# Performance work log

Hardware: AMD Instinct MI355X
Metric: run time of the kernel (lower is better)

The kernel has to match this reference:

```python
import jax, jax.numpy as jnp
import numpy as np

H = 100      # hidden size
L = 4096     # sequence length


def setup_inputs() -> dict:
    key = jax.random.key(0)
    ks = jax.random.split(key, 11)
    s = 1.0 / np.sqrt(H)
    u = lambda k, sh: jax.random.uniform(k, sh, jnp.float32, -s, s)
    return {
        "input_seq": jax.random.normal(ks[0], (L,), jnp.float32),
        "W_ih_l0": u(ks[1], (4 * H, 1)),
        "W_hh_l0": u(ks[2], (4 * H, H)),
        "b_ih_l0": u(ks[3], (4 * H,)),
        "b_hh_l0": u(ks[4], (4 * H,)),
        "W_ih_l1": u(ks[5], (4 * H, H)),
        "W_hh_l1": u(ks[6], (4 * H, H)),
        "b_ih_l1": u(ks[7], (4 * H,)),
        "b_hh_l1": u(ks[8], (4 * H,)),
        "W_lin": u(ks[9], (1, H)),
        "b_lin": u(ks[10], (1,)),
    }


def _lstm_layer(x, Wih, Whh, bih, bhh):
    # x: [L, B, in] -> hs: [L, B, H]. PyTorch gate order: i, f, g, o.
    h_dim = Wih.shape[0] // 4
    b = bih + bhh

    def step(carry, xt):
        h, c = carry
        gates = xt @ Wih.T + h @ Whh.T + b          # [B, 4H]
        i, f, g, o = jnp.split(gates, 4, axis=-1)
        c = jax.nn.sigmoid(f) * c + jax.nn.sigmoid(i) * jnp.tanh(g)
        h = jax.nn.sigmoid(o) * jnp.tanh(c)
        return (h, c), h

    B = x.shape[1]
    h0 = jnp.zeros((B, h_dim), x.dtype)
    c0 = jnp.zeros((B, h_dim), x.dtype)
    _, hs = jax.lax.scan(step, (h0, c0), x)
    return hs


def reference(input_seq, W_ih_l0, W_hh_l0, b_ih_l0, b_hh_l0,
              W_ih_l1, W_hh_l1, b_ih_l1, b_hh_l1, W_lin, b_lin):
    x = input_seq.reshape(-1, 1, 1)                 # [L, B=1, 1]
    h1 = _lstm_layer(x, W_ih_l0, W_hh_l0, b_ih_l0, b_hh_l0)   # [L,1,H]
    h2 = _lstm_layer(h1, W_ih_l1, W_hh_l1, b_ih_l1, b_hh_l1)  # [L,1,H]
    preds = h2.reshape(h2.shape[0], -1) @ W_lin.T + b_lin      # [L,1]
    return preds[-1]                                 # [1]
```

## Files before the change

kernel.cpp:

```cpp
#include <hip/hip_runtime.h>

#define HH 100
#define LL 4096
#define NT 512

#define WS_H1_FLOATS (LL*128)
#define WS_NEEDED ((size_t)WS_H1_FLOATS*4 + (size_t)LL*4)

typedef float v2f __attribute__((ext_vector_type(2)));
__device__ __forceinline__ v2f fma2(v2f a, v2f b, v2f c) { return __builtin_elementwise_fma(a, b, c); }
__device__ __forceinline__ v2f v2c(float2 f) { v2f r; r.x = f.x; r.y = f.y; return r; }

__device__ __forceinline__ float sigmoidf_(float x) { return 1.0f / (1.0f + __expf(-x)); }
__device__ __forceinline__ float tanhf_(float x)    { return 1.0f - 2.0f / (__expf(2.0f * x) + 1.0f); }

#define DECLROW(n) v2f n##_0,n##_1,n##_2,n##_3,n##_4,n##_5,n##_6,n##_7,n##_8,n##_9,n##_10,n##_11, \
                       n##_12,n##_13,n##_14,n##_15,n##_16,n##_17,n##_18,n##_19,n##_20,n##_21,n##_22,n##_23,n##_24;
#define LOADROW(n, P) { const float2* q2_ = reinterpret_cast<const float2*>(P); \
  n##_0=v2c(q2_[0]);   n##_1=v2c(q2_[1]);   n##_2=v2c(q2_[2]);   n##_3=v2c(q2_[3]);   n##_4=v2c(q2_[4]); \
  n##_5=v2c(q2_[5]);   n##_6=v2c(q2_[6]);   n##_7=v2c(q2_[7]);   n##_8=v2c(q2_[8]);   n##_9=v2c(q2_[9]); \
  n##_10=v2c(q2_[10]); n##_11=v2c(q2_[11]); n##_12=v2c(q2_[12]); n##_13=v2c(q2_[13]); n##_14=v2c(q2_[14]); \
  n##_15=v2c(q2_[15]); n##_16=v2c(q2_[16]); n##_17=v2c(q2_[17]); n##_18=v2c(q2_[18]); n##_19=v2c(q2_[19]); \
  n##_20=v2c(q2_[20]); n##_21=v2c(q2_[21]); n##_22=v2c(q2_[22]); n##_23=v2c(q2_[23]); n##_24=v2c(q2_[24]); }

#define STEP2(j,p,q) { float4 hv = hb4[j]; v2f hl, hh; hl.x=hv.x; hl.y=hv.y; hh.x=hv.z; hh.y=hv.w; \
  a0=fma2(wa_##p,hl,a0); a0=fma2(wa_##q,hh,a0); \
  a1=fma2(wb_##p,hl,a1); a1=fma2(wb_##q,hh,a1); }
#define DOT2TAIL { float4 hv = hb4[12]; v2f hl; hl.x = hv.x; hl.y = hv.y; \
  a0 = fma2(wa_24, hl, a0); a1 = fma2(wb_24, hl, a1); }
#define DOT2ALL  STEP2(0,0,1) STEP2(1,2,3) STEP2(2,4,5) STEP2(3,6,7) STEP2(4,8,9) STEP2(5,10,11) \
                 STEP2(6,12,13) STEP2(7,14,15) STEP2(8,16,17) STEP2(9,18,19) STEP2(10,20,21) STEP2(11,22,23) DOT2TAIL

#define WSTEP2(j,p,q) { float4 hv = hb4[j]; v2f hl, hh; hl.x=hv.x; hl.y=hv.y; hh.x=hv.z; hh.y=hv.w; \
  a0=fma2(wc_##p,hl,a0); a0=fma2(wc_##q,hh,a0); \
  a1=fma2(wd_##p,hl,a1); a1=fma2(wd_##q,hh,a1); }
#define WDOT2TAIL { float4 hv = hb4[12]; v2f hl; hl.x = hv.x; hl.y = hv.y; \
  a0 = fma2(wc_24, hl, a0); a1 = fma2(wd_24, hl, a1); }
#define WDOT2ALL WSTEP2(0,0,1) WSTEP2(1,2,3) WSTEP2(2,4,5) WSTEP2(3,6,7) WSTEP2(4,8,9) WSTEP2(5,10,11) \
                 WSTEP2(6,12,13) WSTEP2(7,14,15) WSTEP2(8,16,17) WSTEP2(9,18,19) WSTEP2(10,20,21) WSTEP2(11,22,23) WDOT2TAIL

#define AST(p,v) __hip_atomic_store((p), (v), __ATOMIC_RELAXED, __HIP_MEMORY_SCOPE_AGENT)
#define ALD(p)   __hip_atomic_load((p), __ATOMIC_RELAXED, __HIP_MEMORY_SCOPE_AGENT)
#define AFLAGST(p) __hip_atomic_store((p), 1, __ATOMIC_RELEASE, __HIP_MEMORY_SCOPE_AGENT)
#define AFLAGLD(p) __hip_atomic_load((p), __ATOMIC_ACQUIRE, __HIP_MEMORY_SCOPE_AGENT)

#define P_LDS_FLOATS 5120

__global__ __attribute__((amdgpu_flat_work_group_size(NT, NT)))
           __attribute__((amdgpu_waves_per_eu(2, 2)))
void lstm_pipe2(const float* __restrict__ x_seq,  const float* __restrict__ Wih0,
                const float* __restrict__ Whh0,   const float* __restrict__ bih0,
                const float* __restrict__ bhh0,   const float* __restrict__ Wih1,
                const float* __restrict__ Whh1,   const float* __restrict__ bih1,
                const float* __restrict__ bhh1,   const float* __restrict__ Wlin,
                const float* __restrict__ blin,   float* __restrict__ ws_h1,
                int* __restrict__ ws_flag,        float* __restrict__ out)
{
    extern __shared__ float lds[];
    const int tid = threadIdx.x;

    if (blockIdx.x == 0) {
        float* x_s   = lds;
        float* h1_s  = lds + 4096;
        float* part0 = lds + 4200;

        const int half = tid & 1;
        const int q    = tid >> 1;
        const bool act = (q < 200);
        const int r0   = act ? 2*q : 0;

        {   const float4* src = reinterpret_cast<const float4*>(x_seq);
            float4* dst = reinterpret_cast<float4*>(x_s);
            for (int i = tid; i < LL/4; i += NT) dst[i] = src[i]; }
        if (tid < 104) h1_s[tid] = 0.0f;

        DECLROW(wa) DECLROW(wb)
        LOADROW(wa, Whh0 + (r0+0)*HH + half*50)
        LOADROW(wb, Whh0 + (r0+1)*HH + half*50)
        float bw0 = 0.f, bw1 = 0.f;
        if (act) {
            if (half == 0) { bw0 = bih0[r0] + bhh0[r0]; bw1 = bih0[r0+1] + bhh0[r0+1]; }
            else           { bw0 = Wih0[r0];            bw1 = Wih0[r0+1]; }
        }
        const float4* hb4 = reinterpret_cast<const float4*>(h1_s + half*52);
        float c0 = 0.0f;
        __syncthreads();

        for (int t = 0; t < LL; ++t) {
            const float xt  = x_s[t];
            const float xvs = half ? xt : 1.0f;
            if (act) {
                v2f a0 = {0.f,0.f}, a1 = {0.f,0.f};
                DOT2ALL
                float* pw = part0 + half*400 + r0;
                pw[0] = fmaf(bw0, xvs, a0.x + a0.y);
                pw[1] = fmaf(bw1, xvs, a1.x + a1.y);
            }
            __syncthreads();
            if (tid < 100) {
                const int j = tid;
                float G0 = part0[j]       + part0[400 + j];
                float G1 = part0[j + 100] + part0[500 + j];
                float G2 = part0[j + 200] + part0[600 + j];
                float G3 = part0[j + 300] + part0[700 + j];
                c0 = sigmoidf_(G1)*c0 + sigmoidf_(G0)*tanhf_(G2);
                float h = sigmoidf_(G3)*tanhf_(c0);
                h1_s[j + 2*(j >= 50)] = h;
                AST(&ws_h1[t*128 + j], h);
            }
            __syncthreads();
            if (tid == 0) AFLAGST(&ws_flag[t]);
        }
    } else {
        float* h1c  = lds;
        float* h2_s = lds + 208;
        float* pwhh = lds + 312;
        float* pwih = lds + 1112;
        float* red  = lds + 2712;

        const int half = tid & 1;
        const int q    = tid >> 1;
        const bool act = (q < 200);
        const int r0   = act ? 2*q : 0;

        DECLROW(wa) DECLROW(wb)
        DECLROW(wc) DECLROW(wd)
        LOADROW(wa, Whh1 + (r0+0)*HH + half*50)
        LOADROW(wb, Whh1 + (r0+1)*HH + half*50)
        LOADROW(wc, Wih1 + (r0+0)*HH + half*50)
        LOADROW(wd, Wih1 + (r0+1)*HH + half*50)
        float bw0 = 0.f, bw1 = 0.f;
        if (act && half == 0) { bw0 = bih1[r0] + bhh1[r0]; bw1 = bih1[r0+1] + bhh1[r0+1]; }

        const bool gl = (tid >= 400) && (tid < 500);
        const int  j  = tid - 400;
        const float wl = gl ? Wlin[j] : 0.0f;
        float c1 = 0.0f;

        if (tid < 208) h1c[tid] = 0.0f;
        if (tid < 104) h2_s[tid] = 0.0f;
        __syncthreads();

        if (gl) {
            while (AFLAGLD(&ws_flag[0]) == 0) {}
            h1c[j + 2*(j >= 50)] = ALD(&ws_h1[j]);
            while (AFLAGLD(&ws_flag[1]) == 0) {}
            h1c[104 + j + 2*(j >= 50)] = ALD(&ws_h1[128 + j]);
        }
        __syncthreads();
        if (act) {
            const float4* hb4 = reinterpret_cast<const float4*>(h1c + half*52);
            v2f a0 = {0.f,0.f}, a1 = {0.f,0.f};
            WDOT2ALL
            float* pw = pwih + half*400 + r0;
            pw[0] = a0.x + a0.y + bw0;
            pw[1] = a1.x + a1.y + bw1;
        }
        __syncthreads();

        for (int t = 0; t < LL; ++t) {
            const int cur = t & 1, nxt = cur ^ 1;
            float hnf = 0.0f;

            if (act) {
                const float4* hb4 = reinterpret_cast<const float4*>(h2_s + half*52);
                v2f a0 = {0.f,0.f}, a1 = {0.f,0.f};
                DOT2ALL
                float* pw = pwhh + half*400 + r0;
                pw[0] = a0.x + a0.y;
                pw[1] = a1.x + a1.y;
            }
            if (gl) {
                const int tp2 = (t+2 < LL) ? t+2 : LL-1;
                while (AFLAGLD(&ws_flag[tp2]) == 0) {}
                hnf = ALD(&ws_h1[tp2*128 + j]);
            }
            __syncthreads();

            if (act) {
                const float4* hb4 = reinterpret_cast<const float4*>(h1c + nxt*104 + half*52);
                v2f a0 = {0.f,0.f}, a1 = {0.f,0.f};
                WDOT2ALL
                float* pw = pwih + nxt*800 + half*400 + r0;
                pw[0] = a0.x + a0.y + bw0;
                pw[1] = a1.x + a1.y + bw1;
            }
            if (gl) {
                const float* pc = pwih + cur*800;
                float G0 = (pwhh[j]       + pwhh[400 + j]) + (pc[j]       + pc[400 + j]);
                float G1 = (pwhh[100 + j] + pwhh[500 + j]) + (pc[100 + j] + pc[500 + j]);
                float G2 = (pwhh[200 + j] + pwhh[600 + j]) + (pc[200 + j] + pc[600 + j]);
                float G3 = (pwhh[300 + j] + pwhh[700 + j]) + (pc[300 + j] + pc[700 + j]);
                c1 = sigmoidf_(G1)*c1 + sigmoidf_(G0)*tanhf_(G2);
                h2_s[j + 2*(j >= 50)] = sigmoidf_(G3)*tanhf_(c1);
                h1c[cur*104 + j + 2*(j >= 50)] = hnf;
            }
            __syncthreads();
        }

        if (gl) red[j] = wl * h2_s[j + 2*(j >= 50)];
        __syncthreads();
        if (tid == 0) {
            float s = blin[0];
            for (int k = 0; k < HH; ++k) s += red[k];
            out[0] = s;
        }
    }
}

#define NLDSROW 176
#define RB0  176
#define WQ_OFF   4096
#define H1_OFF   (WQ_OFF + 2*NLDSROW*52)
#define H2_OFF   (H1_OFF + 104)
#define PART_OFF (H2_OFF + 104)
#define Q_OFF    (PART_OFF + 2048)
#define LDS_FLOATS (Q_OFF + 352)

#define STEP4(j,p,q) { float4 hv = hb4[j]; v2f hl, hh; hl.x=hv.x; hl.y=hv.y; hh.x=hv.z; hh.y=hv.w; \
  a0=fma2(wa_##p,hl,a0); a0=fma2(wa_##q,hh,a0); \
  a1=fma2(wb_##p,hl,a1); a1=fma2(wb_##q,hh,a1); \
  a2=fma2(wc_##p,hl,a2); a2=fma2(wc_##q,hh,a2); \
  a3=fma2(wd_##p,hl,a3); a3=fma2(wd_##q,hh,a3); }
#define TSK(j) { float4 wv = tp4[j]; float4 hv = hb4t[j]; v2f wl_,wh_,hl_,hh_; \
  wl_.x=wv.x; wl_.y=wv.y; wh_.x=wv.z; wh_.y=wv.w; hl_.x=hv.x; hl_.y=hv.y; hh_.x=hv.z; hh_.y=hv.w; \
  tq=fma2(wl_,hl_,tq); tq=fma2(wh_,hh_,tq); }

__global__ __attribute__((amdgpu_flat_work_group_size(NT, NT)))
           __attribute__((amdgpu_waves_per_eu(2, 2)))
void lstm_v256_kernel(const float* __restrict__ x_seq, const float* __restrict__ Wih0,
                      const float* __restrict__ Whh0,  const float* __restrict__ bih0,
                      const float* __restrict__ bhh0,  const float* __restrict__ Wih1,
                      const float* __restrict__ Whh1,  const float* __restrict__ bih1,
                      const float* __restrict__ bhh1,  const float* __restrict__ Wlin,
                      const float* __restrict__ blin,  float* __restrict__ out)
{
    extern __shared__ float lds[];
    float* x_s    = lds;
    float* wq     = lds + WQ_OFF;
    float* h1_s   = lds + H1_OFF;
    float* h2_s   = lds + H2_OFF;
    float* part_s = lds + PART_OFF;
    float* q_s    = lds + Q_OFF;

    const int tid  = threadIdx.x;
    const int half = tid & 1;
    const int qid  = tid >> 1;
    const int rowbase = RB0 + 4*qid;

    {   const float4* src = reinterpret_cast<const float4*>(x_seq);
        float4* dst = reinterpret_cast<float4*>(x_s);
        for (int i = tid; i < LL/4; i += NT) dst[i] = src[i]; }
    for (int idx = tid; idx < 2*NLDSROW*50; idx += NT) {
        int hf  = idx / (NLDSROW*50);
        int rem = idx - hf*(NLDSROW*50);
        int row = rem / 50;
        int cc  = rem - row*50;
        wq[(hf*NLDSROW + row)*52 + cc] = Whh0[row*HH + hf*50 + cc];
    }
    if (tid < 104) { h1_s[tid] = 0.0f; h2_s[tid] = 0.0f; }

    const float* M; int r0;
    if (rowbase < 400)      { M = Whh0; r0 = rowbase; }
    else if (rowbase < 800) { M = Wih1; r0 = rowbase - 400; }
    else                    { M = Whh1; r0 = rowbase - 800; }

    DECLROW(wa) DECLROW(wb) DECLROW(wc) DECLROW(wd)
    LOADROW(wa, M + (r0+0)*HH + half*50)
    LOADROW(wb, M + (r0+1)*HH + half*50)
    LOADROW(wc, M + (r0+2)*HH + half*50)
    LOADROW(wd, M + (r0+3)*HH + half*50)

    float bw0, bw1, bw2, bw3;
    {
        const int ra = rowbase, rb = rowbase+1, rc = rowbase+2, rd = rowbase+3;
        if (half == 0) {
            bw0 = (ra < 400) ? (bih0[ra] + bhh0[ra]) : (ra < 800) ? (bih1[ra-400] + bhh1[ra-400]) : 0.0f;
            bw1 = (rb < 400) ? (bih0[rb] + bhh0[rb]) : (rb < 800) ? (bih1[rb-400] + bhh1[rb-400]) : 0.0f;
            bw2 = (rc < 400) ? (bih0[rc] + bhh0[rc]) : (rc < 800) ? (bih1[rc-400] + bhh1[rc-400]) : 0.0f;
            bw3 = (rd < 400) ? (bih0[rd] + bhh0[rd]) : (rd < 800) ? (bih1[rd-400] + bhh1[rd-400]) : 0.0f;
        } else {
            bw0 = (ra < 400) ? Wih0[ra] : 0.0f;
            bw1 = (rb < 400) ? Wih0[rb] : 0.0f;
            bw2 = (rc < 400) ? Wih0[rc] : 0.0f;
            bw3 = (rd < 400) ? Wih0[rd] : 0.0f;
        }
    }

    float lb = 0.0f;
    if (tid < 2*NLDSROW) lb = half ? Wih0[qid] : (bih0[qid] + bhh0[qid]);
    const float4* tp4  = reinterpret_cast<const float4*>(wq + (half*NLDSROW + qid)*52);
    const float4* hb4t = reinterpret_cast<const float4*>(h1_s + half*52);
    const float4* hb4  = reinterpret_cast<const float4*>(((rowbase < 800) ? h1_s : h2_s) + half*52);

    const float wl = (tid < HH) ? Wlin[tid] : 0.0f;
    const int slotbase = qid + half*1024;
    float c0 = 0.0f, c1 = 0.0f;
    __syncthreads();

    for (int t = 0; t <= LL; ++t) {
        const float xt  = x_s[(t < LL) ? t : (LL-1)];
        const float xvs = half ? xt : 1.0f;
        {
            v2f a0 = {0.f,0.f}, a1 = {0.f,0.f}, a2 = {0.f,0.f}, a3 = {0.f,0.f};
            STEP4(0,0,1)   STEP4(1,2,3)   STEP4(2,4,5)   STEP4(3,6,7)
            STEP4(4,8,9)   STEP4(5,10,11) STEP4(6,12,13) STEP4(7,14,15)
            STEP4(8,16,17) STEP4(9,18,19) STEP4(10,20,21) STEP4(11,22,23)
            { float4 hv = hb4[12]; v2f hl; hl.x = hv.x; hl.y = hv.y;
              a0 = fma2(wa_24, hl, a0); a1 = fma2(wb_24, hl, a1);
              a2 = fma2(wc_24, hl, a2); a3 = fma2(wd_24, hl, a3); }
            part_s[slotbase + 0*256] = fmaf(bw0, xvs, a0.x + a0.y);
            part_s[slotbase + 1*256] = fmaf(bw1, xvs, a1.x + a1.y);
            part_s[slotbase + 2*256] = fmaf(bw2, xvs, a2.x + a2.y);
            part_s[slotbase + 3*256] = fmaf(bw3, xvs, a3.x + a3.y);
        }
        if (tid < 2*NLDSROW) {
            v2f tq = {0.f,0.f};
            TSK(0) TSK(1) TSK(2) TSK(3) TSK(4) TSK(5)
            TSK(6) TSK(7) TSK(8) TSK(9) TSK(10) TSK(11)
            { float4 wv = tp4[12]; float4 hv = hb4t[12];
              v2f wl_, hl_; wl_.x = wv.x; wl_.y = wv.y; hl_.x = hv.x; hl_.y = hv.y;
              tq = fma2(wl_, hl_, tq); }
            q_s[qid + half*NLDSROW] = fmaf(lb, xvs, tq.x + tq.y);
        }
        __syncthreads();
        if (tid < HH) {
            const int jj = tid;
            float g[4];
            #pragma unroll
            for (int k = 0; k < 4; ++k) {
                int r = jj + k*100;
                if (r < NLDSROW) g[k] = q_s[r] + q_s[r + NLDSROW];
                else { int rr = r - RB0; int bb = (rr >> 2) + ((rr & 3) << 8);
                       g[k] = part_s[bb] + part_s[bb + 1024]; }
            }
            if (t < LL) {
                c0 = sigmoidf_(g[1])*c0 + sigmoidf_(g[0])*tanhf_(g[2]);
                h1_s[jj + 2*(jj >= 50)] = sigmoidf_(g[3])*tanhf_(c0);
            }
        } else if (tid >= 128 && tid < 128 + HH) {
            if (t >= 1) {
                const int jj = tid - 128;
                float v[4];
                #pragma unroll
                for (int k = 0; k < 4; ++k) {
                    int g1i = jj + k*100;
                    int rr1 = (400 + g1i) - RB0; int b1i = (rr1 >> 2) + ((rr1 & 3) << 8);
                    int rr2 = (800 + g1i) - RB0; int b2i = (rr2 >> 2) + ((rr2 & 3) << 8);
                    v[k] = (part_s[b1i] + part_s[b1i + 1024]) + (part_s[b2i] + part_s[b2i + 1024]);
                }
                c1 = sigmoidf_(v[1])*c1 + sigmoidf_(v[0])*tanhf_(v[2]);
                h2_s[jj + 2*(jj >= 50)] = sigmoidf_(v[3])*tanhf_(c1);
            }
        }
        __syncthreads();
    }
    if (tid < HH) part_s[tid] = wl * h2_s[tid + 2*(tid >= 50)];
    __syncthreads();
    if (tid == 0) {
        float s = 0.0f;
        for (int k = 0; k < HH; ++k) s += part_s[k];
        out[0] = s + blin[0];
    }
}

extern "C" void kernel_launch(void* const* d_in, const int* in_sizes, int n_in,
                              void* d_out, int out_size, void* d_ws, size_t ws_size,
                              hipStream_t stream) {
    (void)in_sizes; (void)n_in; (void)out_size;

    const float* x_seq = (const float*)d_in[0];
    const float* Wih0  = (const float*)d_in[1];
    const float* Whh0  = (const float*)d_in[2];
    const float* bih0  = (const float*)d_in[3];
    const float* bhh0  = (const float*)d_in[4];
    const float* Wih1  = (const float*)d_in[5];
    const float* Whh1  = (const float*)d_in[6];
    const float* bih1  = (const float*)d_in[7];
    const float* bhh1  = (const float*)d_in[8];
    const float* Wlin  = (const float*)d_in[9];
    const float* blin  = (const float*)d_in[10];
    float* out = (float*)d_out;

    if (d_ws != nullptr && ws_size >= WS_NEEDED) {
        float* ws_h1  = (float*)d_ws;
        int*   ws_flg = (int*)((char*)d_ws + (size_t)WS_H1_FLOATS*4);
        hipMemsetAsync(ws_flg, 0, LL*sizeof(int), stream);
        hipLaunchKernelGGL(lstm_pipe2, dim3(2), dim3(NT),
                           P_LDS_FLOATS*sizeof(float), stream,
                           x_seq, Wih0, Whh0, bih0, bhh0,
                           Wih1, Whh1, bih1, bhh1, Wlin, blin,
                           ws_h1, ws_flg, out);
    } else {
        static bool attr_set = false;
        if (!attr_set) {
            hipFuncSetAttribute((const void*)lstm_v256_kernel,
                                hipFuncAttributeMaxDynamicSharedMemorySize,
                                LDS_FLOATS * (int)sizeof(float));
            attr_set = true;
        }
        hipLaunchKernelGGL(lstm_v256_kernel, dim3(1), dim3(NT),
                           LDS_FLOATS * sizeof(float), stream,
                           x_seq, Wih0, Whh0, bih0, bhh0,
                           Wih1, Whh1, bih1, bhh1, Wlin, blin, out);
    }
}
```

Before: 4.575 ms.

## Replicate gate math per wave to drop one barrier per LSTM step

Both blocks of the two-block pipelined LSTM are restructured so each wave computes the gate nonlinearities redundantly for its 50-element half and writes h into a private per-wave LDS buffer. It then immediately runs the next step's matvec. Partial sums are double-buffered, so only one __syncthreads per timestep remains instead of two. Layer 2 splits its waves into a Whh class and a Wih class with four rows per thread. The aim is to cut barrier and serialization latency on the recurrence critical path, at the cost of redundant transcendental work and more LDS.

```diff
diff --git a/kernel.cpp b/kernel.cpp
--- a/kernel.cpp
+++ b/kernel.cpp
@@ -23,182 +23,208 @@
   n##_15=v2c(q2_[15]); n##_16=v2c(q2_[16]); n##_17=v2c(q2_[17]); n##_18=v2c(q2_[18]); n##_19=v2c(q2_[19]); \
   n##_20=v2c(q2_[20]); n##_21=v2c(q2_[21]); n##_22=v2c(q2_[22]); n##_23=v2c(q2_[23]); n##_24=v2c(q2_[24]); }
 
-#define STEP2(j,p,q) { float4 hv = hb4[j]; v2f hl, hh; hl.x=hv.x; hl.y=hv.y; hh.x=hv.z; hh.y=hv.w; \
-  a0=fma2(wa_##p,hl,a0); a0=fma2(wa_##q,hh,a0); \
-  a1=fma2(wb_##p,hl,a1); a1=fma2(wb_##q,hh,a1); }
-#define DOT2TAIL { float4 hv = hb4[12]; v2f hl; hl.x = hv.x; hl.y = hv.y; \
-  a0 = fma2(wa_24, hl, a0); a1 = fma2(wb_24, hl, a1); }
+#define STEP2(j,p,q) { float4 hv = hb4[j]; v2f hlo, hhi; hlo.x=hv.x; hlo.y=hv.y; hhi.x=hv.z; hhi.y=hv.w; \
+  a0=fma2(wa_##p,hlo,a0); a0=fma2(wa_##q,hhi,a0); \
+  a1=fma2(wb_##p,hlo,a1); a1=fma2(wb_##q,hhi,a1); }
 #define DOT2ALL  STEP2(0,0,1) STEP2(1,2,3) STEP2(2,4,5) STEP2(3,6,7) STEP2(4,8,9) STEP2(5,10,11) \
-                 STEP2(6,12,13) STEP2(7,14,15) STEP2(8,16,17) STEP2(9,18,19) STEP2(10,20,21) STEP2(11,22,23) DOT2TAIL
-
-#define WSTEP2(j,p,q) { float4 hv = hb4[j]; v2f hl, hh; hl.x=hv.x; hl.y=hv.y; hh.x=hv.z; hh.y=hv.w; \
-  a0=fma2(wc_##p,hl,a0); a0=fma2(wc_##q,hh,a0); \
-  a1=fma2(wd_##p,hl,a1); a1=fma2(wd_##q,hh,a1); }
-#define WDOT2TAIL { float4 hv = hb4[12]; v2f hl; hl.x = hv.x; hl.y = hv.y; \
-  a0 = fma2(wc_24, hl, a0); a1 = fma2(wd_24, hl, a1); }
-#define WDOT2ALL WSTEP2(0,0,1) WSTEP2(1,2,3) WSTEP2(2,4,5) WSTEP2(3,6,7) WSTEP2(4,8,9) WSTEP2(5,10,11) \
-                 WSTEP2(6,12,13) WSTEP2(7,14,15) WSTEP2(8,16,17) WSTEP2(9,18,19) WSTEP2(10,20,21) WSTEP2(11,22,23) WDOT2TAIL
+                 STEP2(6,12,13) STEP2(7,14,15) STEP2(8,16,17) STEP2(9,18,19) STEP2(10,20,21) STEP2(11,22,23) \
+                 { float4 hv = hb4[12]; v2f hlo; hlo.x=hv.x; hlo.y=hv.y; \
+                   a0=fma2(wa_24,hlo,a0); a1=fma2(wb_24,hlo,a1); }
+
+#define STEP4(j,p,q) { float4 hv = hb4[j]; v2f hlo, hhi; hlo.x=hv.x; hlo.y=hv.y; hhi.x=hv.z; hhi.y=hv.w; \
+  a0=fma2(wa_##p,hlo,a0); a0=fma2(wa_##q,hhi,a0); \
+  a1=fma2(wb_##p,hlo,a1); a1=fma2(wb_##q,hhi,a1); \
+  a2=fma2(wc_##p,hlo,a2); a2=fma2(wc_##q,hhi,a2); \
+  a3=fma2(wd_##p,hlo,a3); a3=fma2(wd_##q,hhi,a3); }
+#define DOT4ALL  STEP4(0,0,1) STEP4(1,2,3) STEP4(2,4,5) STEP4(3,6,7) STEP4(4,8,9) STEP4(5,10,11) \
+                 STEP4(6,12,13) STEP4(7,14,15) STEP4(8,16,17) STEP4(9,18,19) STEP4(10,20,21) STEP4(11,22,23) \
+                 { float4 hv = hb4[12]; v2f hlo; hlo.x=hv.x; hlo.y=hv.y; \
+                   a0=fma2(wa_24,hlo,a0); a1=fma2(wb_24,hlo,a1); \
+                   a2=fma2(wc_24,hlo,a2); a3=fma2(wd_24,hlo,a3); }
 
 #define AST(p,v) __hip_atomic_store((p), (v), __ATOMIC_RELAXED, __HIP_MEMORY_SCOPE_AGENT)
 #define ALD(p)   __hip_atomic_load((p), __ATOMIC_RELAXED, __HIP_MEMORY_SCOPE_AGENT)
 #define AFLAGST(p) __hip_atomic_store((p), 1, __ATOMIC_RELEASE, __HIP_MEMORY_SCOPE_AGENT)
 #define AFLAGLD(p) __hip_atomic_load((p), __ATOMIC_ACQUIRE, __HIP_MEMORY_SCOPE_AGENT)
 
-#define P_LDS_FLOATS 5120
+#define P_LDS_FLOATS 6400
 
 __global__ __attribute__((amdgpu_flat_work_group_size(NT, NT)))
            __attribute__((amdgpu_waves_per_eu(2, 2)))
-void lstm_pipe2(const float* __restrict__ x_seq,  const float* __restrict__ Wih0,
-                const float* __restrict__ Whh0,   const float* __restrict__ bih0,
-                const float* __restrict__ bhh0,   const float* __restrict__ Wih1,
-                const float* __restrict__ Whh1,   const float* __restrict__ bih1,
-                const float* __restrict__ bhh1,   const float* __restrict__ Wlin,
-                const float* __restrict__ blin,   float* __restrict__ ws_h1,
-                int* __restrict__ ws_flag,        float* __restrict__ out)
+void lstm_pipe2b(const float* __restrict__ x_seq,  const float* __restrict__ Wih0,
+                 const float* __restrict__ Whh0,   const float* __restrict__ bih0,
+                 const float* __restrict__ bhh0,   const float* __restrict__ Wih1,
+                 const float* __restrict__ Whh1,   const float* __restrict__ bih1,
+                 const float* __restrict__ bhh1,   const float* __restrict__ Wlin,
+                 const float* __restrict__ blin,   float* __restrict__ ws_h1,
+                 int* __restrict__ ws_flag,        float* __restrict__ out)
 {
     extern __shared__ float lds[];
-    const int tid = threadIdx.x;
+    const int tid  = threadIdx.x;
+    const int lane = tid & 63;
+    const int wid  = tid >> 6;
 
     if (blockIdx.x == 0) {
-        float* x_s   = lds;
-        float* h1_s  = lds + 4096;
-        float* part0 = lds + 4200;
-
-        const int half = tid & 1;
-        const int q    = tid >> 1;
-        const bool act = (q < 200);
-        const int r0   = act ? 2*q : 0;
+        float* x_s  = lds;
+        float* hbuf = lds + 4096;
+        float* part = lds + 4544;
+
+        const int hf = wid >> 2;
+        const int u  = (wid & 3)*64 + lane;
+        const bool act = (u < 200);
+        const int r0 = act ? 2*u : 0;
 
         {   const float4* src = reinterpret_cast<const float4*>(x_seq);
             float4* dst = reinterpret_cast<float4*>(x_s);
             for (int i = tid; i < LL/4; i += NT) dst[i] = src[i]; }
-        if (tid < 104) h1_s[tid] = 0.0f;
+        for (int i = tid; i < 448 + 1600; i += NT) lds[4096 + i] = 0.0f;
 
         DECLROW(wa) DECLROW(wb)
-        LOADROW(wa, Whh0 + (r0+0)*HH + half*50)
-        LOADROW(wb, Whh0 + (r0+1)*HH + half*50)
+        LOADROW(wa, Whh0 + (r0+0)*HH + hf*50)
+        LOADROW(wb, Whh0 + (r0+1)*HH + hf*50)
         float bw0 = 0.f, bw1 = 0.f;
         if (act) {
-            if (half == 0) { bw0 = bih0[r0] + bhh0[r0]; bw1 = bih0[r0+1] + bhh0[r0+1]; }
-            else           { bw0 = Wih0[r0];            bw1 = Wih0[r0+1]; }
-        }
-        const float4* hb4 = reinterpret_cast<const float4*>(h1_s + half*52);
+            if (hf == 0) { bw0 = bih0[r0] + bhh0[r0]; bw1 = bih0[r0+1] + bhh0[r0+1]; }
+            else         { bw0 = Wih0[r0];            bw1 = Wih0[r0+1]; }
+        }
+
+        float* hb = hbuf + wid*56;
+        const float4* hb4 = reinterpret_cast<const float4*>(hb);
+        const int e = hf*50 + ((lane < 50) ? lane : 49);
         float c0 = 0.0f;
         __syncthreads();
 
-        for (int t = 0; t < LL; ++t) {
-            const float xt  = x_s[t];
-            const float xvs = half ? xt : 1.0f;
+        {
+            const float xvs = hf ? x_s[0] : 1.0f;
             if (act) {
                 v2f a0 = {0.f,0.f}, a1 = {0.f,0.f};
                 DOT2ALL
-                float* pw = part0 + half*400 + r0;
+                float* pw = part + hf*400 + r0;
                 pw[0] = fmaf(bw0, xvs, a0.x + a0.y);
                 pw[1] = fmaf(bw1, xvs, a1.x + a1.y);
             }
-            __syncthreads();
-            if (tid < 100) {
-                const int j = tid;
-                float G0 = part0[j]       + part0[400 + j];
-                float G1 = part0[j + 100] + part0[500 + j];
-                float G2 = part0[j + 200] + part0[600 + j];
-                float G3 = part0[j + 300] + part0[700 + j];
+        }
+        __syncthreads();
+
+        for (int t = 0; t < LL; ++t) {
+            if (tid == 0 && t > 0) AFLAGST(&ws_flag[t-1]);
+            const float* pr = part + (t & 1)*800;
+            if (lane < 50) {
+                float G0 = pr[e]       + pr[400 + e];
+                float G1 = pr[100 + e] + pr[500 + e];
+                float G2 = pr[200 + e] + pr[600 + e];
+                float G3 = pr[300 + e] + pr[700 + e];
                 c0 = sigmoidf_(G1)*c0 + sigmoidf_(G0)*tanhf_(G2);
                 float h = sigmoidf_(G3)*tanhf_(c0);
-                h1_s[j + 2*(j >= 50)] = h;
-                AST(&ws_h1[t*128 + j], h);
-            }
-            __syncthreads();
-            if (tid == 0) AFLAGST(&ws_flag[t]);
-        }
-    } else {
-        float* h1c  = lds;
-        float* h2_s = lds + 208;
-        float* pwhh = lds + 312;
-        float* pwih = lds + 1112;
-        float* red  = lds + 2712;
-
-        const int half = tid & 1;
-        const int q    = tid >> 1;
-        const bool act = (q < 200);
-        const int r0   = act ? 2*q : 0;
-
-        DECLROW(wa) DECLROW(wb)
-        DECLROW(wc) DECLROW(wd)
-        LOADROW(wa, Whh1 + (r0+0)*HH + half*50)
-        LOADROW(wb, Whh1 + (r0+1)*HH + half*50)
-        LOADROW(wc, Wih1 + (r0+0)*HH + half*50)
-        LOADROW(wd, Wih1 + (r0+1)*HH + half*50)
-        float bw0 = 0.f, bw1 = 0.f;
-        if (act && half == 0) { bw0 = bih1[r0] + bhh1[r0]; bw1 = bih1[r0+1] + bhh1[r0+1]; }
-
-        const bool gl = (tid >= 400) && (tid < 500);
-        const int  j  = tid - 400;
-        const float wl = gl ? Wlin[j] : 0.0f;
-        float c1 = 0.0f;
-
-        if (tid < 208) h1c[tid] = 0.0f;
-        if (tid < 104) h2_s[tid] = 0.0f;
-        __syncthreads();
-
-        if (gl) {
-            while (AFLAGLD(&ws_flag[0]) == 0) {}
-            h1c[j + 2*(j >= 50)] = ALD(&ws_h1[j]);
-            while (AFLAGLD(&ws_flag[1]) == 0) {}
-            h1c[104 + j + 2*(j >= 50)] = ALD(&ws_h1[128 + j]);
-        }
-        __syncthreads();
-        if (act) {
-            const float4* hb4 = reinterpret_cast<const float4*>(h1c + half*52);
-            v2f a0 = {0.f,0.f}, a1 = {0.f,0.f};
-            WDOT2ALL
-            float* pw = pwih + half*400 + r0;
-            pw[0] = a0.x + a0.y + bw0;
-            pw[1] = a1.x + a1.y + bw1;
-        }
-        __syncthreads();
-
-        for (int t = 0; t < LL; ++t) {
-            const int cur = t & 1, nxt = cur ^ 1;
-            float hnf = 0.0f;
-
+                hb[lane] = h;
+                if (wid == 0 || wid == 4) AST(&ws_h1[t*128 + e], h);
+            }
+            asm volatile("" ::: "memory");
+            const int  t1  = (t+1 < LL) ? t+1 : LL-1;
+            const float xvs = hf ? x_s[t1] : 1.0f;
             if (act) {
-                const float4* hb4 = reinterpret_cast<const float4*>(h2_s + half*52);
                 v2f a0 = {0.f,0.f}, a1 = {0.f,0.f};
                 DOT2ALL
-                float* pw = pwhh + half*400 + r0;
-                pw[0] = a0.x + a0.y;
-                pw[1] = a1.x + a1.y;
-            }
-            if (gl) {
-                const int tp2 = (t+2 < LL) ? t+2 : LL-1;
-                while (AFLAGLD(&ws_flag[tp2]) == 0) {}
-                hnf = ALD(&ws_h1[tp2*128 + j]);
+                float* pw = part + ((t+1) & 1)*800 + hf*400 + r0;
+                pw[0] = fmaf(bw0, xvs, a0.x + a0.y);
+                pw[1] = fmaf(bw1, xvs, a1.x + a1.y);
             }
             __syncthreads();
-
+        }
+        if (tid == 0) AFLAGST(&ws_flag[LL-1]);
+    } else {
+        float* hbuf = lds;
+        float* part = lds + 448;
+        float* red  = lds + 3648;
+
+        const int cls = wid >> 2;
+        const int hf  = (wid >> 1) & 1;
+        const int uu  = (wid & 1)*64 + lane;
+        const bool act = (uu < 100);
+        const int r0 = act ? 4*uu : 0;
+        const float* mat = (cls == 0) ? Whh1 : Wih1;
+
+        DECLROW(wa) DECLROW(wb) DECLROW(wc) DECLROW(wd)
+        LOADROW(wa, mat + (r0+0)*HH + hf*50)
+        LOADROW(wb, mat + (r0+1)*HH + hf*50)
+        LOADROW(wc, mat + (r0+2)*HH + hf*50)
+        LOADROW(wd, mat + (r0+3)*HH + hf*50)
+        float bw0 = 0.f, bw1 = 0.f, bw2 = 0.f, bw3 = 0.f;
+        if (act && cls == 1 && hf == 0) {
+            bw0 = bih1[r0]   + bhh1[r0];
+            bw1 = bih1[r0+1] + bhh1[r0+1];
+            bw2 = bih1[r0+2] + bhh1[r0+2];
+            bw3 = bih1[r0+3] + bhh1[r0+3];
+        }
+
+        float* hb = hbuf + wid*56;
+        const float4* hb4 = reinterpret_cast<const float4*>(hb);
+        const int e = hf*50 + ((lane < 50) ? lane : 49);
+        const float wl = (lane < 50) ? Wlin[e] : 0.0f;
+
+        float c1 = 0.0f, h2_lane = 0.0f, h1_next = 0.0f;
+
+        for (int i = tid; i < 448 + 3200 + 104; i += NT) lds[i] = 0.0f;
+        __syncthreads();
+
+        if (cls == 1) {
+            if (lane < 50) {
+                while (AFLAGLD(&ws_flag[0]) == 0) {}
+                hb[lane] = ALD(&ws_h1[e]);
+            }
+            asm volatile("" ::: "memory");
             if (act) {
-                const float4* hb4 = reinterpret_cast<const float4*>(h1c + nxt*104 + half*52);
-                v2f a0 = {0.f,0.f}, a1 = {0.f,0.f};
-                WDOT2ALL
-                float* pw = pwih + nxt*800 + half*400 + r0;
-                pw[0] = a0.x + a0.y + bw0;
-                pw[1] = a1.x + a1.y + bw1;
-            }
-            if (gl) {
-                const float* pc = pwih + cur*800;
-                float G0 = (pwhh[j]       + pwhh[400 + j]) + (pc[j]       + pc[400 + j]);
-                float G1 = (pwhh[100 + j] + pwhh[500 + j]) + (pc[100 + j] + pc[500 + j]);
-                float G2 = (pwhh[200 + j] + pwhh[600 + j]) + (pc[200 + j] + pc[600 + j]);
-                float G3 = (pwhh[300 + j] + pwhh[700 + j]) + (pc[300 + j] + pc[700 + j]);
-                c1 = sigmoidf_(G1)*c1 + sigmoidf_(G0)*tanhf_(G2);
-                h2_s[j + 2*(j >= 50)] = sigmoidf_(G3)*tanhf_(c1);
-                h1c[cur*104 + j + 2*(j >= 50)] = hnf;
+                v2f a0 = {0.f,0.f}, a1 = {0.f,0.f}, a2 = {0.f,0.f}, a3 = {0.f,0.f};
+                DOT4ALL
+                reinterpret_cast<float4*>(part + hf*400 + r0)[0] =
+                    make_float4(a0.x+a0.y+bw0, a1.x+a1.y+bw1, a2.x+a2.y+bw2, a3.x+a3.y+bw3);
+            }
+            if (lane < 50) {
+                while (AFLAGLD(&ws_flag[1]) == 0) {}
+                h1_next = ALD(&ws_h1[128 + e]);
+            }
+        }
+        __syncthreads();
+
+        for (int t = 0; t < LL; ++t) {
+            const float* pr  = part + (t & 1)*1600;
+            float*       pwn = part + ((t+1) & 1)*1600;
+            if (cls == 0) {
+                if (lane < 50) {
+                    float G0 = (pr[e]       + pr[400 + e]) + (pr[800 + e]        + pr[1200 + e]);
+                    float G1 = (pr[100 + e] + pr[500 + e]) + (pr[800 + 100 + e]  + pr[1300 + e]);
+                    float G2 = (pr[200 + e] + pr[600 + e]) + (pr[800 + 200 + e]  + pr[1400 + e]);
+                    float G3 = (pr[300 + e] + pr[700 + e]) + (pr[800 + 300 + e]  + pr[1500 + e]);
+                    c1 = sigmoidf_(G1)*c1 + sigmoidf_(G0)*tanhf_(G2);
+                    h2_lane = sigmoidf_(G3)*tanhf_(c1);
+                    hb[lane] = h2_lane;
+                }
+                asm volatile("" ::: "memory");
+                if (act) {
+                    v2f a0 = {0.f,0.f}, a1 = {0.f,0.f}, a2 = {0.f,0.f}, a3 = {0.f,0.f};
+                    DOT4ALL
+                    reinterpret_cast<float4*>(pwn + 800 + hf*400 + r0)[0] =
+                        make_float4(a0.x+a0.y, a1.x+a1.y, a2.x+a2.y, a3.x+a3.y);
+                }
+            } else {
+                if (lane < 50) hb[lane] = h1_next;
+                asm volatile("" ::: "memory");
+                if (act) {
+                    v2f a0 = {0.f,0.f}, a1 = {0.f,0.f}, a2 = {0.f,0.f}, a3 = {0.f,0.f};
+                    DOT4ALL
+                    reinterpret_cast<float4*>(pwn + hf*400 + r0)[0] =
+                        make_float4(a0.x+a0.y+bw0, a1.x+a1.y+bw1, a2.x+a2.y+bw2, a3.x+a3.y+bw3);
+                }
+                if (lane < 50) {
+                    const int tp2 = (t+2 < LL) ? t+2 : LL-1;
+                    while (AFLAGLD(&ws_flag[tp2]) == 0) {}
+                    h1_next = ALD(&ws_h1[tp2*128 + e]);
+                }
             }
             __syncthreads();
         }
 
-        if (gl) red[j] = wl * h2_s[j + 2*(j >= 50)];
+        if (cls == 0 && (wid & 1) == 0 && lane < 50) red[e] = wl * h2_lane;
         __syncthreads();
         if (tid == 0) {
             float s = blin[0];
@@ -217,11 +243,6 @@
 #define Q_OFF    (PART_OFF + 2048)
 #define LDS_FLOATS (Q_OFF + 352)
 
-#define STEP4(j,p,q) { float4 hv = hb4[j]; v2f hl, hh; hl.x=hv.x; hl.y=hv.y; hh.x=hv.z; hh.y=hv.w; \
-  a0=fma2(wa_##p,hl,a0); a0=fma2(wa_##q,hh,a0); \
-  a1=fma2(wb_##p,hl,a1); a1=fma2(wb_##q,hh,a1); \
-  a2=fma2(wc_##p,hl,a2); a2=fma2(wc_##q,hh,a2); \
-  a3=fma2(wd_##p,hl,a3); a3=fma2(wd_##q,hh,a3); }
 #define TSK(j) { float4 wv = tp4[j]; float4 hv = hb4t[j]; v2f wl_,wh_,hl_,hh_; \
   wl_.x=wv.x; wl_.y=wv.y; wh_.x=wv.z; wh_.y=wv.w; hl_.x=hv.x; hl_.y=hv.y; hh_.x=hv.z; hh_.y=hv.w; \
   tq=fma2(wl_,hl_,tq); tq=fma2(wh_,hh_,tq); }
@@ -252,11 +273,11 @@
         float4* dst = reinterpret_cast<float4*>(x_s);
         for (int i = tid; i < LL/4; i += NT) dst[i] = src[i]; }
     for (int idx = tid; idx < 2*NLDSROW*50; idx += NT) {
-        int hf  = idx / (NLDSROW*50);
-        int rem = idx - hf*(NLDSROW*50);
+        int hfx = idx / (NLDSROW*50);
+        int rem = idx - hfx*(NLDSROW*50);
         int row = rem / 50;
         int cc  = rem - row*50;
-        wq[(hf*NLDSROW + row)*52 + cc] = Whh0[row*HH + hf*50 + cc];
+        wq[(hfx*NLDSROW + row)*52 + cc] = Whh0[row*HH + hfx*50 + cc];
     }
     if (tid < 104) { h1_s[tid] = 0.0f; h2_s[tid] = 0.0f; }
 
@@ -303,12 +324,7 @@
         const float xvs = half ? xt : 1.0f;
         {
             v2f a0 = {0.f,0.f}, a1 = {0.f,0.f}, a2 = {0.f,0.f}, a3 = {0.f,0.f};
-            STEP4(0,0,1)   STEP4(1,2,3)   STEP4(2,4,5)   STEP4(3,6,7)
-            STEP4(4,8,9)   STEP4(5,10,11) STEP4(6,12,13) STEP4(7,14,15)
-            STEP4(8,16,17) STEP4(9,18,19) STEP4(10,20,21) STEP4(11,22,23)
-            { float4 hv = hb4[12]; v2f hl; hl.x = hv.x; hl.y = hv.y;
-              a0 = fma2(wa_24, hl, a0); a1 = fma2(wb_24, hl, a1);
-              a2 = fma2(wc_24, hl, a2); a3 = fma2(wd_24, hl, a3); }
+            DOT4ALL
             part_s[slotbase + 0*256] = fmaf(bw0, xvs, a0.x + a0.y);
             part_s[slotbase + 1*256] = fmaf(bw1, xvs, a1.x + a1.y);
             part_s[slotbase + 2*256] = fmaf(bw2, xvs, a2.x + a2.y);
@@ -386,7 +402,7 @@
         float* ws_h1  = (float*)d_ws;
         int*   ws_flg = (int*)((char*)d_ws + (size_t)WS_H1_FLOATS*4);
         hipMemsetAsync(ws_flg, 0, LL*sizeof(int), stream);
-        hipLaunchKernelGGL(lstm_pipe2, dim3(2), dim3(NT),
+        hipLaunchKernelGGL(lstm_pipe2b, dim3(2), dim3(NT),
                            P_LDS_FLOATS*sizeof(float), stream,
                            x_seq, Wih0, Whh0, bih0, bhh0,
                            Wih1, Whh1, bih1, bhh1, Wlin, blin,
```

Result: no change. 4.567 ms (-0.2%).
